# Kernel optimization log

Measured on AMD Instinct MI355X. Metric: run time of the kernel, lower is better.

The kernel has to match this reference:

```python
import jax, jax.numpy as jnp
import numpy as np

B, T, C = 4, 4096, 1024
HS = 64


def setup_inputs() -> dict:
    key = jax.random.key(0)
    k0, k1, k2, k3 = jax.random.split(key, 4)
    std = 1.0 / np.sqrt(C)
    return {
        "x": jax.random.normal(k0, (B, T, C), dtype=jnp.float32),
        "Wk": jax.random.normal(k1, (HS, C), dtype=jnp.float32) * std,
        "Wq": jax.random.normal(k2, (HS, C), dtype=jnp.float32) * std,
        "Wv": jax.random.normal(k3, (HS, C), dtype=jnp.float32) * std,
        "i": 0,
        "embed_dim": 1024,
        "head_size_sel": 64,
    }


def reference(x, Wk, Wq, Wv, i, embed_dim, head_size_sel):
    # NAS slicing of inputs/weights (static ints -> jit-safe)
    xs = x[:, :, :embed_dim]                      # [B,T,E]
    kw = Wk[:head_size_sel, :embed_dim]           # [H,E]
    qw = Wq[:head_size_sel, :embed_dim]
    vw = Wv[:head_size_sel, :embed_dim]
    k = jnp.einsum('bte,he->bth', xs, kw)         # [B,T,H]
    q = jnp.einsum('bte,he->bth', xs, qw)
    v = jnp.einsum('bte,he->bth', xs, vw)
    scale = jnp.asarray(head_size_sel, x.dtype) ** -0.5
    wei = jnp.einsum('bqh,bkh->bqk', q, k) * scale  # [B,T,T] full score matrix
    Tlen = x.shape[1]
    causal = jnp.tril(jnp.ones((Tlen, Tlen), dtype=bool))
    wei = jnp.where(causal[None, :, :], wei, -jnp.inf)
    wei = jax.nn.softmax(wei, axis=-1)
    # dropout: eval mode (identity) for deterministic reference
    out = jnp.einsum('bqk,bkh->bqh', wei, v)      # [B,T,H]
    return out
```

## Files before the change

### kernel.cpp

```cpp
#include <hip/hip_runtime.h>
#include <math.h>

typedef __bf16 bf16_t;
typedef __bf16 bf16x8 __attribute__((ext_vector_type(8)));
typedef __bf16 bf16x4 __attribute__((ext_vector_type(4)));
typedef float  floatx4 __attribute__((ext_vector_type(4)));

#define TT   4096
#define CD   1024
#define HSZ  64
#define NROW 16384
#define NEG_BIG (-1e30f)

#define WB_OFF 0
#define Q_OFF  196608
#define K_OFF  (196608 + NROW * HSZ)
#define V_OFF  (196608 + 2 * NROW * HSZ)

#if __has_builtin(__builtin_amdgcn_exp2f)
__device__ __forceinline__ float fexp2(float x) { return __builtin_amdgcn_exp2f(x); }
#else
__device__ __forceinline__ float fexp2(float x) { return exp2f(x); }
#endif

__device__ __forceinline__ float qmax(float v) {
  v = fmaxf(v, __shfl_xor(v, 16));
  v = fmaxf(v, __shfl_xor(v, 32));
  return v;
}
__device__ __forceinline__ float qsum(float v) {
  v += __shfl_xor(v, 16);
  v += __shfl_xor(v, 32);
  return v;
}

__global__ __launch_bounds__(256, 1) void wcvt_kernel(
    const float* __restrict__ Wk, const float* __restrict__ Wq,
    const float* __restrict__ Wv, bf16_t* __restrict__ Wb)
{
  const int t    = blockIdx.x * 256 + threadIdx.x;
  const int e    = t * 4;
  const int tile = e >> 9;
  const int kc   = tile / 12;
  const int t12  = tile - kc * 12;
  const int r    = e & 511;
  const int lane = r >> 3;
  const int j0   = r & 7;
  const int wsel = t12 >> 2;
  const int nt   = t12 & 3;
  const int n    = nt * 16 + (lane & 15);
  const int k    = kc * 32 + (lane >> 4) * 8 + j0;
  const float* src = (wsel == 0) ? Wq : (wsel == 1) ? Wk : Wv;
  float4 f = *(const float4*)(src + n * CD + k);
  bf16x4 o;
  o[0] = (bf16_t)f.x; o[1] = (bf16_t)f.y; o[2] = (bf16_t)f.z; o[3] = (bf16_t)f.w;
  *(bf16x4*)(Wb + e) = o;
}

__global__ __launch_bounds__(512, 4) void qkv_proj_kernel(
    const float* __restrict__ x, const bf16_t* __restrict__ Wb,
    bf16_t* __restrict__ qg, bf16_t* __restrict__ kfr, bf16_t* __restrict__ vfr)
{
  const int tid  = threadIdx.x;
  const int lane = tid & 63;
  const int wave = tid >> 6;
  const int mt   = wave >> 2;
  const int tg   = wave & 3;
  const int mr   = lane & 15;
  const int quad = lane >> 4;
  const int m0   = blockIdx.x * 32 + mt * 16;

  floatx4 acc[3];
#pragma unroll
  for (int i = 0; i < 3; ++i) acc[i] = (floatx4){0.f, 0.f, 0.f, 0.f};

  const float* xp = x + (size_t)(m0 + mr) * CD + quad * 8;
  const bf16_t* wp0 = Wb + tg * 3 * 512 + lane * 8;

#pragma unroll 4
  for (int kc = 0; kc < 32; ++kc) {
    float4 xa = *(const float4*)(xp + kc * 32);
    float4 xb = *(const float4*)(xp + kc * 32 + 4);
    const bf16_t* wp = wp0 + kc * 6144;
    bf16x8 wf0 = *(const bf16x8*)(wp);
    bf16x8 wf1 = *(const bf16x8*)(wp + 512);
    bf16x8 wf2 = *(const bf16x8*)(wp + 1024);
    bf16x8 af;
    af[0]=(bf16_t)xa.x; af[1]=(bf16_t)xa.y; af[2]=(bf16_t)xa.z; af[3]=(bf16_t)xa.w;
    af[4]=(bf16_t)xb.x; af[5]=(bf16_t)xb.y; af[6]=(bf16_t)xb.z; af[7]=(bf16_t)xb.w;
    acc[0] = __builtin_amdgcn_mfma_f32_16x16x32_bf16(af, wf0, acc[0], 0, 0, 0);
    acc[1] = __builtin_amdgcn_mfma_f32_16x16x32_bf16(af, wf1, acc[1], 0, 0, 0);
    acc[2] = __builtin_amdgcn_mfma_f32_16x16x32_bf16(af, wf2, acc[2], 0, 0, 0);
  }

  const float qscale = 0.18033688011112042f;
#pragma unroll
  for (int i = 0; i < 3; ++i) {
    const int t12  = tg * 3 + i;
    const int wsel = t12 >> 2;
    const int nt   = t12 & 3;
#pragma unroll
    for (int r = 0; r < 4; ++r) {
      const int trow = m0 + quad * 4 + r;
      const int h    = nt * 16 + mr;
      const float v  = acc[i][r];
      if (wsel == 0) {
        qg[(size_t)trow * HSZ + h] = (bf16_t)(v * qscale);
      } else if (wsel == 1) {
        const size_t a = ((((size_t)(trow >> 6)) * 4 + ((trow >> 4) & 3)) * 2
                          + (h >> 5)) * 512
                         + ((h >> 3) & 3) * 128 + (trow & 15) * 8 + (h & 7);
        kfr[a] = (bf16_t)v;
      } else {
        const size_t a = ((((size_t)(trow >> 6)) * 2 + ((trow >> 5) & 1)) * 4
                          + (h >> 4)) * 512
                         + ((trow >> 3) & 3) * 128 + (h & 15) * 8 + (trow & 7);
        vfr[a] = (bf16_t)v;
      }
    }
  }
}

__device__ __forceinline__ void softmax_step(
    floatx4 (&sv)[4], float& mstv, float& lstv, floatx4 (&ov)[4],
    bf16_t* plp, const int mr, const int quad)
{
  float a = fmaxf(fmaxf(sv[0][0], sv[0][1]), fmaxf(sv[0][2], sv[0][3]));
  float b = fmaxf(fmaxf(sv[1][0], sv[1][1]), fmaxf(sv[1][2], sv[1][3]));
  float c = fmaxf(fmaxf(sv[2][0], sv[2][1]), fmaxf(sv[2][2], sv[2][3]));
  float d = fmaxf(fmaxf(sv[3][0], sv[3][1]), fmaxf(sv[3][2], sv[3][3]));
  float mx = fmaxf(fmaxf(a, b), fmaxf(c, d));
  mx = qmax(mx);
  const float mnew = fmaxf(mstv, mx);
  float rs = 0.f;
#pragma unroll
  for (int nt = 0; nt < 4; ++nt) {
    const float p0 = fexp2(sv[nt][0] - mnew);
    const float p1 = fexp2(sv[nt][1] - mnew);
    const float p2 = fexp2(sv[nt][2] - mnew);
    const float p3 = fexp2(sv[nt][3] - mnew);
    rs += (p0 + p1) + (p2 + p3);
    bf16x4 w;
    w[0] = (bf16_t)p0; w[1] = (bf16_t)p1; w[2] = (bf16_t)p2; w[3] = (bf16_t)p3;
    *(bf16x4*)(plp + mr * 72 + nt * 16 + quad * 4) = w;
  }
  if (__all(mx <= mstv)) {
    lstv += rs;
  } else {
    const float alpha = fexp2(mstv - mnew);
    mstv = mnew;
    lstv = alpha * lstv + rs;
#pragma unroll
    for (int nt = 0; nt < 4; ++nt)
#pragma unroll
      for (int r = 0; r < 4; ++r) ov[nt][r] *= alpha;
  }
}

__global__ __launch_bounds__(1024, 4) void attn_kernel(
    const bf16_t* __restrict__ qg, const bf16_t* __restrict__ kfr,
    const bf16_t* __restrict__ vfr, float* __restrict__ out)
{
  __shared__ __align__(16) char smem[73728];
  __shared__ float cml[16][16][2];
  bf16_t* plds = (bf16_t*)smem;
  float (*cmbo)[16][68] = (float (*)[16][68])smem;

  const int tid  = threadIdx.x;
  const int lane = tid & 63;
  const int wave = tid >> 6;
  const int mr   = lane & 15;
  const int quad = lane >> 4;

  const int bid = blockIdx.x;
  const int b   = bid & 3;
  const int pr  = bid >> 2;
  const int gA  = pr;
  const int gB  = 127 - pr;
  const int nAw = (gA >> 1) + 1;
  const int nBw = (gB >> 1) + 1;
  int na = (16 * nAw + ((nAw + nBw) >> 1)) / (nAw + nBw);
  na = na < 1 ? 1 : (na > 15 ? 15 : na);

  const bool inA   = wave < na;
  const int g      = inA ? gA : gB;
  const int slot   = inA ? wave : wave - na;
  const int nsplit = inA ? na : 16 - na;
  const int q0     = g * 32;
  const int ktmax  = g >> 1;

  const size_t baseq = (size_t)b * TT * HSZ;
  const bf16_t* kb = kfr + (size_t)b * 64 * 4096;
  const bf16_t* vb = vfr + (size_t)b * 64 * 4096;

  bf16_t* pl0 = plds + wave * 2304;
  bf16_t* pl1 = pl0 + 1152;

  bf16x8 qf[2][2];
#pragma unroll
  for (int s = 0; s < 2; ++s) {
    const bf16_t* qp = qg + baseq + (size_t)(q0 + s * 16 + mr) * HSZ + quad * 8;
    qf[s][0] = *(const bf16x8*)qp;
    qf[s][1] = *(const bf16x8*)(qp + 32);
  }

  floatx4 o0[4], o1[4];
#pragma unroll
  for (int i = 0; i < 4; ++i) {
    o0[i] = (floatx4){0.f, 0.f, 0.f, 0.f};
    o1[i] = (floatx4){0.f, 0.f, 0.f, 0.f};
  }
  float mst[2] = {NEG_BIG, NEG_BIG};
  float lst[2] = {0.f, 0.f};

  for (int kt = slot; kt <= ktmax; kt += nsplit) {
    const int k0 = kt * 64;

    floatx4 s0[4], s1[4];
#pragma unroll
    for (int i = 0; i < 4; ++i) {
      s0[i] = (floatx4){0.f, 0.f, 0.f, 0.f};
      s1[i] = (floatx4){0.f, 0.f, 0.f, 0.f};
    }
#pragma unroll
    for (int nt = 0; nt < 4; ++nt) {
      const bf16_t* kp = kb + ((size_t)kt * 4 + nt) * 1024 + lane * 8;
      bf16x8 kb0 = *(const bf16x8*)kp;
      bf16x8 kb1 = *(const bf16x8*)(kp + 512);
      s0[nt] = __builtin_amdgcn_mfma_f32_16x16x32_bf16(kb0, qf[0][0], s0[nt], 0, 0, 0);
      s0[nt] = __builtin_amdgcn_mfma_f32_16x16x32_bf16(kb1, qf[0][1], s0[nt], 0, 0, 0);
      s1[nt] = __builtin_amdgcn_mfma_f32_16x16x32_bf16(kb0, qf[1][0], s1[nt], 0, 0, 0);
      s1[nt] = __builtin_amdgcn_mfma_f32_16x16x32_bf16(kb1, qf[1][1], s1[nt], 0, 0, 0);
    }

    if (kt == ktmax) {
      const int qa0 = q0 + mr;
#pragma unroll
      for (int nt = 0; nt < 4; ++nt) {
#pragma unroll
        for (int r = 0; r < 4; ++r) {
          const int kv = k0 + nt * 16 + quad * 4 + r;
          if (kv > qa0)      s0[nt][r] = NEG_BIG;
          if (kv > qa0 + 16) s1[nt][r] = NEG_BIG;
        }
      }
    }

    softmax_step(s0, mst[0], lst[0], o0, pl0, mr, quad);

    bf16x8 vfa[4];
#pragma unroll
    for (int nt = 0; nt < 4; ++nt)
      vfa[nt] = *(const bf16x8*)(vb + ((size_t)kt * 8 + nt) * 512 + lane * 8);

    softmax_step(s1, mst[1], lst[1], o1, pl1, mr, quad);

    bf16x8 vfb[4];
#pragma unroll
    for (int nt = 0; nt < 4; ++nt)
      vfb[nt] = *(const bf16x8*)(vb + ((size_t)kt * 8 + nt) * 512 + 2048 + lane * 8);

    {
      bf16x8 pa0 = *(bf16x8*)&pl0[mr * 72 + quad * 8];
      bf16x8 pa1 = *(bf16x8*)&pl1[mr * 72 + quad * 8];
#pragma unroll
      for (int nt = 0; nt < 4; ++nt) {
        o0[nt] = __builtin_amdgcn_mfma_f32_16x16x32_bf16(vfa[nt], pa0, o0[nt], 0, 0, 0);
        o1[nt] = __builtin_amdgcn_mfma_f32_16x16x32_bf16(vfa[nt], pa1, o1[nt], 0, 0, 0);
      }
      bf16x8 pb0 = *(bf16x8*)&pl0[mr * 72 + 32 + quad * 8];
      bf16x8 pb1 = *(bf16x8*)&pl1[mr * 72 + 32 + quad * 8];
#pragma unroll
      for (int nt = 0; nt < 4; ++nt) {
        o0[nt] = __builtin_amdgcn_mfma_f32_16x16x32_bf16(vfb[nt], pb0, o0[nt], 0, 0, 0);
        o1[nt] = __builtin_amdgcn_mfma_f32_16x16x32_bf16(vfb[nt], pb1, o1[nt], 0, 0, 0);
      }
    }
  }

  __syncthreads();
#pragma unroll
  for (int s = 0; s < 2; ++s) {
    const float lsum = qsum(lst[s]);
    if (lane < 16) {
      cml[wave][lane][0] = mst[s];
      cml[wave][lane][1] = lsum;
    }
    __syncthreads();
    {
      const int lo = inA ? 0 : na;
      const int hi = inA ? na : 16;
      float mstar = cml[lo][mr][0];
      for (int i = lo + 1; i < hi; ++i) mstar = fmaxf(mstar, cml[i][mr][0]);
      const float scale = fexp2(mst[s] - mstar);
#pragma unroll
      for (int nt = 0; nt < 4; ++nt) {
        floatx4 t;
#pragma unroll
        for (int r = 0; r < 4; ++r) t[r] = (s ? o1[nt][r] : o0[nt][r]) * scale;
        *(floatx4*)&cmbo[wave][mr][nt * 16 + quad * 4] = t;
      }
    }
    __syncthreads();
    {
      const int grp = tid >> 9;
      const int row = (tid >> 5) & 15;
      const int c0  = (tid & 31) * 2;
      const int lo  = grp ? na : 0;
      const int hi  = grp ? 16 : na;
      const int gq0 = (grp ? gB : gA) * 32 + s * 16;
      float mstar = cml[lo][row][0];
      for (int i = lo + 1; i < hi; ++i) mstar = fmaxf(mstar, cml[i][row][0]);
      float l = 0.f;
      for (int i = lo; i < hi; ++i)
        l += cml[i][row][1] * fexp2(cml[i][row][0] - mstar);
      float sx = 0.f, sy = 0.f;
      for (int i = lo; i < hi; ++i) {
        float2 v = *(float2*)&cmbo[i][row][c0];
        sx += v.x; sy += v.y;
      }
      const float invl = 1.0f / l;
      float2 res; res.x = sx * invl; res.y = sy * invl;
      *(float2*)(out + baseq + (size_t)(gq0 + row) * HSZ + c0) = res;
    }
    __syncthreads();
  }
}

extern "C" void kernel_launch(void* const* d_in, const int* in_sizes, int n_in,
                              void* d_out, int out_size, void* d_ws, size_t ws_size,
                              hipStream_t stream) {
  const float* x  = (const float*)d_in[0];
  const float* Wk = (const float*)d_in[1];
  const float* Wq = (const float*)d_in[2];
  const float* Wv = (const float*)d_in[3];
  float* out = (float*)d_out;

  bf16_t* ws  = (bf16_t*)d_ws;
  bf16_t* Wb  = ws + WB_OFF;
  bf16_t* qg  = ws + Q_OFF;
  bf16_t* kfr = ws + K_OFF;
  bf16_t* vfr = ws + V_OFF;

  wcvt_kernel<<<dim3(192), dim3(256), 0, stream>>>(Wk, Wq, Wv, Wb);
  qkv_proj_kernel<<<dim3(512), dim3(512), 0, stream>>>(x, Wb, qg, kfr, vfr);
  attn_kernel<<<dim3(256), dim3(1024), 0, stream>>>(qg, kfr, vfr, out);
}
```

Baseline: 167.0 us.

## Split QKV projection along K across waves with LDS reduction

The QKV projection kernel now splits the reduction dimension across four wave groups, each computing all 12 output tiles over a quarter of K, instead of splitting the output tiles across waves. Each x fragment is loaded and converted to bf16 once per wave rather than four times, which cuts redundant global reads of x. Partial sums are combined through shared memory followed by a block barrier. This adds LDS usage of about 72KB per block, more accumulator registers, and a serialized epilogue on one quarter of the waves, all of which may reduce occupancy.

```diff
diff --git a/kernel.cpp b/kernel.cpp
--- a/kernel.cpp
+++ b/kernel.cpp
@@ -61,61 +61,71 @@
     const float* __restrict__ x, const bf16_t* __restrict__ Wb,
     bf16_t* __restrict__ qg, bf16_t* __restrict__ kfr, bf16_t* __restrict__ vfr)
 {
+  __shared__ __align__(16) floatx4 red[3][2][12][64];
+
   const int tid  = threadIdx.x;
   const int lane = tid & 63;
   const int wave = tid >> 6;
-  const int mt   = wave >> 2;
-  const int tg   = wave & 3;
+  const int kh   = wave >> 1;
+  const int mt   = wave & 1;
   const int mr   = lane & 15;
   const int quad = lane >> 4;
   const int m0   = blockIdx.x * 32 + mt * 16;
 
-  floatx4 acc[3];
-#pragma unroll
-  for (int i = 0; i < 3; ++i) acc[i] = (floatx4){0.f, 0.f, 0.f, 0.f};
+  floatx4 acc[12];
+#pragma unroll
+  for (int i = 0; i < 12; ++i) acc[i] = (floatx4){0.f, 0.f, 0.f, 0.f};
 
   const float* xp = x + (size_t)(m0 + mr) * CD + quad * 8;
-  const bf16_t* wp0 = Wb + tg * 3 * 512 + lane * 8;
-
-#pragma unroll 4
-  for (int kc = 0; kc < 32; ++kc) {
+
+  for (int kc = kh * 8; kc < kh * 8 + 8; ++kc) {
     float4 xa = *(const float4*)(xp + kc * 32);
     float4 xb = *(const float4*)(xp + kc * 32 + 4);
-    const bf16_t* wp = wp0 + kc * 6144;
-    bf16x8 wf0 = *(const bf16x8*)(wp);
-    bf16x8 wf1 = *(const bf16x8*)(wp + 512);
-    bf16x8 wf2 = *(const bf16x8*)(wp + 1024);
+    const bf16_t* wp = Wb + kc * 6144 + lane * 8;
     bf16x8 af;
     af[0]=(bf16_t)xa.x; af[1]=(bf16_t)xa.y; af[2]=(bf16_t)xa.z; af[3]=(bf16_t)xa.w;
     af[4]=(bf16_t)xb.x; af[5]=(bf16_t)xb.y; af[6]=(bf16_t)xb.z; af[7]=(bf16_t)xb.w;
-    acc[0] = __builtin_amdgcn_mfma_f32_16x16x32_bf16(af, wf0, acc[0], 0, 0, 0);
-    acc[1] = __builtin_amdgcn_mfma_f32_16x16x32_bf16(af, wf1, acc[1], 0, 0, 0);
-    acc[2] = __builtin_amdgcn_mfma_f32_16x16x32_bf16(af, wf2, acc[2], 0, 0, 0);
-  }
-
-  const float qscale = 0.18033688011112042f;
-#pragma unroll
-  for (int i = 0; i < 3; ++i) {
-    const int t12  = tg * 3 + i;
-    const int wsel = t12 >> 2;
-    const int nt   = t12 & 3;
-#pragma unroll
-    for (int r = 0; r < 4; ++r) {
-      const int trow = m0 + quad * 4 + r;
-      const int h    = nt * 16 + mr;
-      const float v  = acc[i][r];
-      if (wsel == 0) {
-        qg[(size_t)trow * HSZ + h] = (bf16_t)(v * qscale);
-      } else if (wsel == 1) {
-        const size_t a = ((((size_t)(trow >> 6)) * 4 + ((trow >> 4) & 3)) * 2
-                          + (h >> 5)) * 512
-                         + ((h >> 3) & 3) * 128 + (trow & 15) * 8 + (h & 7);
-        kfr[a] = (bf16_t)v;
-      } else {
-        const size_t a = ((((size_t)(trow >> 6)) * 2 + ((trow >> 5) & 1)) * 4
-                          + (h >> 4)) * 512
-                         + ((trow >> 3) & 3) * 128 + (h & 15) * 8 + (trow & 7);
-        vfr[a] = (bf16_t)v;
+#pragma unroll
+    for (int i = 0; i < 12; ++i) {
+      bf16x8 wf = *(const bf16x8*)(wp + i * 512);
+      acc[i] = __builtin_amdgcn_mfma_f32_16x16x32_bf16(af, wf, acc[i], 0, 0, 0);
+    }
+  }
+
+  if (kh != 0) {
+#pragma unroll
+    for (int i = 0; i < 12; ++i)
+      red[kh - 1][mt][i][lane] = acc[i];
+  }
+  __syncthreads();
+  if (kh == 0) {
+    const float qscale = 0.18033688011112042f;
+#pragma unroll
+    for (int i = 0; i < 12; ++i) {
+      floatx4 a = acc[i];
+      a += red[0][mt][i][lane];
+      a += red[1][mt][i][lane];
+      a += red[2][mt][i][lane];
+      const int wsel = i >> 2;
+      const int nt   = i & 3;
+#pragma unroll
+      for (int r = 0; r < 4; ++r) {
+        const int trow = m0 + quad * 4 + r;
+        const int h    = nt * 16 + mr;
+        const float v  = a[r];
+        if (wsel == 0) {
+          qg[(size_t)trow * HSZ + h] = (bf16_t)(v * qscale);
+        } else if (wsel == 1) {
+          const size_t adr = ((((size_t)(trow >> 6)) * 4 + ((trow >> 4) & 3)) * 2
+                              + (h >> 5)) * 512
+                             + ((h >> 3) & 3) * 128 + (trow & 15) * 8 + (h & 7);
+          kfr[adr] = (bf16_t)v;
+        } else {
+          const size_t adr = ((((size_t)(trow >> 6)) * 2 + ((trow >> 5) & 1)) * 4
+                              + (h >> 4)) * 512
+                             + ((trow >> 3) & 3) * 128 + (h & 15) * 8 + (trow & 7);
+          vfr[adr] = (bf16_t)v;
+        }
       }
     }
   }
```

Result: faster. 149.9 us (-10.2%).
